# Kernel tuning notes

Measured on AMD Instinct MI355X. Metric: run time of the kernel, lower is better.

Reference implementation:

```python
import jax, jax.numpy as jnp
import numpy as np

NUM_Q = 8
DIM = 256
N_EMBED = 1024
COMMITMENT = 1.0


def setup_inputs() -> dict:
    key = jax.random.key(0)
    kx, ke = jax.random.split(key)
    x = jax.random.normal(kx, (32, 2048, DIM), dtype=jnp.float32)
    # one codebook per residual layer, stored as [dim, n_embed] like torch buffer `embed`
    embeds = jax.random.normal(ke, (NUM_Q, DIM, N_EMBED), dtype=jnp.float32)
    return {"x": x, "embeds": embeds}


def _vq_layer(residual, embed):
    # residual: [B, T, D]; embed: [D, K]
    flat = residual.reshape(-1, DIM)                                   # [N, D]
    dist = (jnp.sum(flat * flat, axis=1, keepdims=True)
            - 2.0 * flat @ embed
            + jnp.sum(embed * embed, axis=0, keepdims=True))           # [N, K]
    ind = jnp.argmin(dist, axis=1)                                     # [N]
    quantize = jnp.take(embed.T, ind, axis=0).reshape(residual.shape)  # [B, T, D]
    # commitment loss: mse(stopgrad(quantize), input)
    loss = jnp.mean((jax.lax.stop_gradient(quantize) - residual) ** 2) * COMMITMENT
    # straight-through estimator
    quantize_st = residual + jax.lax.stop_gradient(quantize - residual)
    # perplexity from code usage histogram
    counts = jnp.zeros((N_EMBED,), dtype=flat.dtype).at[ind].add(1.0)
    avg_probs = counts / flat.shape[0]
    perplexity = jnp.exp(-jnp.sum(avg_probs * jnp.log(avg_probs + 1e-10)))
    return quantize_st, loss, perplexity


def reference(x, embeds):
    def step(carry, embed):
        residual, quantized_out = carry
        q, loss, perp = _vq_layer(residual, embed)
        return (residual - q, quantized_out + q), (loss, perp)

    init = (x, jnp.zeros_like(x))
    (residual, quantized_out), (losses, perps) = jax.lax.scan(step, init, embeds)
    return quantized_out, losses, perps
```

## Files before the change

kernel.cpp:

```cpp
#include <hip/hip_runtime.h>
#include <math.h>
#include <stdint.h>

#define NQ 8
#define DIMV 256
#define KCODES 1024
#define NTOK 65536
#define NELEM (NTOK * DIMV)
#define TOKPB 64

typedef _Float16 f16x8 __attribute__((ext_vector_type(8)));
typedef float    f32x16 __attribute__((ext_vector_type(16)));

__device__ __forceinline__ int rotl3(int s) { return ((s << 3) | (s >> 2)) & 31; }

__global__ __launch_bounds__(256)
void vq_transpose(const float* __restrict__ embeds, float* __restrict__ embedT) {
    const int idx = blockIdx.x * 256 + threadIdx.x;
    const int q   = idx >> 18;
    const int rem = idx & 262143;
    const int k   = rem >> 8;
    const int d   = rem & 255;
    embedT[idx] = embeds[q * 262144 + d * 1024 + k];
}

__global__ __launch_bounds__(256)
void vq_e2(const float* __restrict__ embeds, float* __restrict__ e2) {
    const int idx = blockIdx.x * 256 + threadIdx.x;
    const int q = idx >> 10;
    const int k = idx & 1023;
    const float* e = embeds + q * 262144 + k;
    float s = 0.f;
    for (int d = 0; d < DIMV; ++d) {
        const float v = e[d * 1024];
        s += v * v;
    }
    e2[idx] = s;
}

__global__ __launch_bounds__(256)
void vq_embedB(const float* __restrict__ embeds, _Float16* __restrict__ embedB) {
    const int idx = blockIdx.x * 256 + threadIdx.x;
    const int j    = idx & 7;
    const int s    = (idx >> 3) & 127;
    const int part = (idx >> 10) & 1;
    const int w    = (idx >> 11) & 15;
    const int c    = (idx >> 15) & 15;
    const int q    = idx >> 19;
    const int h  = s >> 6;
    const int cl = s & 63;
    const int d  = c * 16 + h * 8 + j;
    const int k  = w * 64 + cl;
    const float v = embeds[q * 262144 + d * 1024 + k];
    const _Float16 hi = (_Float16)v;
    embedB[idx] = (part == 0) ? hi : (_Float16)(v - (float)hi);
}

#define LDS_BYTES 74080

__global__ __launch_bounds__(512, 4)
void vq_fused(const float* __restrict__ x, float* __restrict__ out,
              const float* __restrict__ embedT, const float* __restrict__ e2,
              const _Float16* __restrict__ embedB,
              float* __restrict__ lossSum, int* __restrict__ counts) {
    extern __shared__ char smem[];
    _Float16* Ahi = (_Float16*)smem;
    _Float16* Alo = (_Float16*)(smem + 32768);
    float* bestS   = (float*)(smem + 65536);
    int*   bestI   = (int*)(smem + 67616);
    int*   indF    = (int*)(smem + 69696);
    float* lossRed = (float*)(smem + 69952);
    float* e2Lds   = (float*)(smem + 69984);

    const int tid    = threadIdx.x;
    const int wave   = tid >> 6;
    const int lane   = tid & 63;
    const int l32    = lane & 31;
    const int h32    = lane >> 5;
    const int tok0   = blockIdx.x * TOKPB;

#pragma unroll
    for (int k = 0; k < 4; ++k) {
        const int si = tid + k * 512;
        const int t  = si >> 5;
        const int s  = si & 31;
        const float4 v0 = *(const float4*)(x + (tok0 + t) * 256 + s * 8);
        const float4 v1 = *(const float4*)(x + (tok0 + t) * 256 + s * 8 + 4);
        const float vv[8] = {v0.x, v0.y, v0.z, v0.w, v1.x, v1.y, v1.z, v1.w};
        f16x8 h8, l8;
#pragma unroll
        for (int e = 0; e < 8; ++e) {
            const _Float16 hi = (_Float16)vv[e];
            h8[e] = hi;
            l8[e] = (_Float16)(vv[e] - (float)hi);
        }
        const int ss = rotl3(s) ^ (t & 31);
        ((f16x8*)(Ahi + t * 256))[ss] = h8;
        ((f16x8*)(Alo + t * 256))[ss] = l8;
    }

#pragma unroll 1
    for (int q = 0; q < NQ; ++q) {
        const _Float16* embedBq = embedB + q * 524288;
        const float*    embedTq = embedT + q * (KCODES * DIMV);

        e2Lds[tid]       = e2[q * KCODES + tid];
        e2Lds[tid + 512] = e2[q * KCODES + tid + 512];
        __syncthreads();

        float bsv0 = 3.4e38f, bsv1 = 3.4e38f;
        int   biv0 = 0x7fffffff, biv1 = 0x7fffffff;

#pragma unroll
        for (int p = 0; p < 4; ++p) {
            f32x16 acc[2];
#pragma unroll
            for (int tt = 0; tt < 2; ++tt)
#pragma unroll
                for (int r = 0; r < 16; ++r) acc[tt][r] = 0.f;

            const char* gBp = (const char*)embedBq + (2 * wave + (p >> 1)) * 4096
                              + (p & 1) * 512 + h32 * 1024 + l32 * 16;

            f16x8 bH[3], bL[3];
            bH[0] = *(const f16x8*)(gBp);
            bL[0] = *(const f16x8*)(gBp + 2048);
            bH[1] = *(const f16x8*)(gBp + 65536);
            bL[1] = *(const f16x8*)(gBp + 65536 + 2048);

#pragma unroll
            for (int c = 0; c < 16; ++c) {
                const int cs = c % 3;
                if (c < 14) {
                    const char* gBn = gBp + (c + 2) * 65536;
                    bH[(c + 2) % 3] = *(const f16x8*)(gBn);
                    bL[(c + 2) % 3] = *(const f16x8*)(gBn + 2048);
                }
                f16x8 aH[2], aL[2];
#pragma unroll
                for (int tt = 0; tt < 2; ++tt) {
                    const int t  = tt * 32 + l32;
                    const int ss = rotl3(2 * c + h32) ^ l32;
                    aH[tt] = ((const f16x8*)(Ahi + t * 256))[ss];
                    aL[tt] = ((const f16x8*)(Alo + t * 256))[ss];
                }
#pragma unroll
                for (int tt = 0; tt < 2; ++tt) {
                    acc[tt] = __builtin_amdgcn_mfma_f32_32x32x16_f16(
                        bH[cs], aH[tt], acc[tt], 0, 0, 0);
                    acc[tt] = __builtin_amdgcn_mfma_f32_32x32x16_f16(
                        bL[cs], aH[tt], acc[tt], 0, 0, 0);
                    acc[tt] = __builtin_amdgcn_mfma_f32_32x32x16_f16(
                        bH[cs], aL[tt], acc[tt], 0, 0, 0);
                }
            }

#pragma unroll
            for (int tt = 0; tt < 2; ++tt) {
                float bs = (tt == 0) ? bsv0 : bsv1;
                int   bi = (tt == 0) ? biv0 : biv1;
#pragma unroll
                for (int r = 0; r < 16; ++r) {
                    const int cd = wave * 128 + p * 32 + (r & 3) + 8 * (r >> 2) + 4 * h32;
                    const float sc = e2Lds[cd] - 2.0f * acc[tt][r];
                    if (sc < bs || (sc == bs && cd < bi)) { bs = sc; bi = cd; }
                }
                if (tt == 0) { bsv0 = bs; biv0 = bi; } else { bsv1 = bs; biv1 = bi; }
            }
        }

#pragma unroll
        for (int tt = 0; tt < 2; ++tt) {
            float bs = (tt == 0) ? bsv0 : bsv1;
            int   bi = (tt == 0) ? biv0 : biv1;
            const float so = __shfl_xor(bs, 32);
            const int   io = __shfl_xor(bi, 32);
            if (so < bs || (so == bs && io < bi)) { bs = so; bi = io; }
            if (h32 == 0) {
                bestS[wave * 65 + tt * 32 + l32] = bs;
                bestI[wave * 65 + tt * 32 + l32] = bi;
            }
        }
        __syncthreads();

        {
            const int t = tid >> 3;
            const int g = tid & 7;
            float bs = bestS[g * 65 + t];
            int   bi = bestI[g * 65 + t];
#pragma unroll
            for (int m = 1; m < 8; m <<= 1) {
                const float so = __shfl_xor(bs, m);
                const int   io = __shfl_xor(bi, m);
                if (so < bs || (so == bs && io < bi)) { bs = so; bi = io; }
            }
            if (g == 0) {
                indF[t] = bi;
                atomicAdd(&counts[q * KCODES + bi], 1);
            }
        }
        __syncthreads();

        {
            const int tl = tid >> 3;
            const int sg = tid & 7;
            const int csel = indF[tl];
            const float* gq = embedTq + csel * 256;
            float lp = 0.f;
            f16x8* rowH = (f16x8*)(Ahi + tl * 256);
            f16x8* rowL = (f16x8*)(Alo + tl * 256);
#pragma unroll
            for (int it = 0; it < 4; ++it) {
                const int slotIdx = sg * 4 + it;
                const int slot = rotl3(slotIdx) ^ (tl & 31);
                f16x8 h8 = rowH[slot];
                f16x8 l8 = rowL[slot];
                const float4 q0 = *(const float4*)(gq + slotIdx * 8);
                const float4 q1 = *(const float4*)(gq + slotIdx * 8 + 4);
                const float qv[8] = {q0.x, q0.y, q0.z, q0.w, q1.x, q1.y, q1.z, q1.w};
#pragma unroll
                for (int e = 0; e < 8; ++e) {
                    const float rv = (float)h8[e] + (float)l8[e];
                    const float nr = rv - qv[e];
                    lp += nr * nr;
                    const _Float16 nh = (_Float16)nr;
                    h8[e] = nh;
                    l8[e] = (_Float16)(nr - (float)nh);
                }
                rowH[slot] = h8;
                rowL[slot] = l8;
            }
#pragma unroll
            for (int off = 32; off > 0; off >>= 1) lp += __shfl_down(lp, off);
            if (lane == 0) lossRed[wave] = lp;
        }
        __syncthreads();
        if (tid < 64) {
            float v = (lane < 8) ? lossRed[lane] : 0.f;
#pragma unroll
            for (int off = 4; off > 0; off >>= 1) v += __shfl_down(v, off);
            if (lane == 0) atomicAdd(lossSum + q, v);
        }
    }

#pragma unroll
    for (int k = 0; k < 4; ++k) {
        const int si = tid + k * 512;
        const int t  = si >> 5;
        const int s  = si & 31;
        const int ss = rotl3(s) ^ (t & 31);
        const f16x8 h8 = ((const f16x8*)(Ahi + t * 256))[ss];
        const f16x8 l8 = ((const f16x8*)(Alo + t * 256))[ss];
        const float4 x0 = *(const float4*)(x + (tok0 + t) * 256 + s * 8);
        const float4 x1 = *(const float4*)(x + (tok0 + t) * 256 + s * 8 + 4);
        float4 o0, o1;
        o0.x = x0.x - ((float)h8[0] + (float)l8[0]);
        o0.y = x0.y - ((float)h8[1] + (float)l8[1]);
        o0.z = x0.z - ((float)h8[2] + (float)l8[2]);
        o0.w = x0.w - ((float)h8[3] + (float)l8[3]);
        o1.x = x1.x - ((float)h8[4] + (float)l8[4]);
        o1.y = x1.y - ((float)h8[5] + (float)l8[5]);
        o1.z = x1.z - ((float)h8[6] + (float)l8[6]);
        o1.w = x1.w - ((float)h8[7] + (float)l8[7]);
        *(float4*)(out + (tok0 + t) * 256 + s * 8)     = o0;
        *(float4*)(out + (tok0 + t) * 256 + s * 8 + 4) = o1;
    }
}

__global__ __launch_bounds__(256)
void vq_finalize(const int* __restrict__ counts, const float* __restrict__ lossSum,
                 float* __restrict__ outTail) {
    const int q = blockIdx.x;
    const int tid = threadIdx.x;
    float s = 0.f;
    for (int k = tid; k < KCODES; k += 256) {
        const float p = (float)counts[q * KCODES + k] * (1.0f / 65536.0f);
        s += p * logf(p + 1e-10f);
    }
    for (int off = 32; off > 0; off >>= 1) s += __shfl_down(s, off);
    __shared__ float wpart[4];
    if ((tid & 63) == 0) wpart[tid >> 6] = s;
    __syncthreads();
    if (tid == 0) {
        outTail[q]     = lossSum[q] * (1.0f / 16777216.0f);
        outTail[8 + q] = expf(-(wpart[0] + wpart[1] + wpart[2] + wpart[3]));
    }
}

extern "C" void kernel_launch(void* const* d_in, const int* in_sizes, int n_in,
                              void* d_out, int out_size, void* d_ws, size_t ws_size,
                              hipStream_t stream) {
    const float* x      = (const float*)d_in[0];
    const float* embeds = (const float*)d_in[1];
    float* out = (float*)d_out;

    float* embedT   = (float*)d_ws;
    float* e2       = embedT + 2097152;
    float* lossSum  = e2 + 8192;
    int*   counts   = (int*)(lossSum + 8);
    _Float16* embedB = (_Float16*)(counts + 8192);

    hipMemsetAsync(lossSum, 0, (8 + 8192) * sizeof(float), stream);

    vq_transpose<<<8192, 256, 0, stream>>>(embeds, embedT);
    vq_e2<<<32, 256, 0, stream>>>(embeds, e2);
    vq_embedB<<<16384, 256, 0, stream>>>(embeds, embedB);

    hipFuncSetAttribute((const void*)vq_fused,
                        hipFuncAttributeMaxDynamicSharedMemorySize, LDS_BYTES);
    vq_fused<<<NTOK / TOKPB, 512, LDS_BYTES, stream>>>(
        x, out, embedT, e2, embedB, lossSum, counts);

    vq_finalize<<<NQ, 256, 0, stream>>>(counts, lossSum, out + NELEM);
}
```

Measured before the change: 1.189 ms.

## Merge argmin and residual-update phases, deepen B prefetch, remap block order

```diff
diff --git a/kernel.cpp b/kernel.cpp
--- a/kernel.cpp
+++ b/kernel.cpp
@@ -56,7 +56,7 @@
     embedB[idx] = (part == 0) ? hi : (_Float16)(v - (float)hi);
 }
 
-#define LDS_BYTES 74080
+#define LDS_BYTES 73792
 
 __global__ __launch_bounds__(512, 4)
 void vq_fused(const float* __restrict__ x, float* __restrict__ out,
@@ -68,16 +68,16 @@
     _Float16* Alo = (_Float16*)(smem + 32768);
     float* bestS   = (float*)(smem + 65536);
     int*   bestI   = (int*)(smem + 67616);
-    int*   indF    = (int*)(smem + 69696);
-    float* lossRed = (float*)(smem + 69952);
-    float* e2Lds   = (float*)(smem + 69984);
+    float* e2Lds   = (float*)(smem + 69696);
 
     const int tid    = threadIdx.x;
     const int wave   = tid >> 6;
     const int lane   = tid & 63;
     const int l32    = lane & 31;
     const int h32    = lane >> 5;
-    const int tok0   = blockIdx.x * TOKPB;
+    const int bid0 = blockIdx.x;
+    const int bid  = ((bid0 & 7) << 7) | (bid0 >> 3);
+    const int tok0 = bid * TOKPB;
 
 #pragma unroll
     for (int k = 0; k < 4; ++k) {
@@ -122,19 +122,21 @@
             const char* gBp = (const char*)embedBq + (2 * wave + (p >> 1)) * 4096
                               + (p & 1) * 512 + h32 * 1024 + l32 * 16;
 
-            f16x8 bH[3], bL[3];
+            f16x8 bH[4], bL[4];
             bH[0] = *(const f16x8*)(gBp);
             bL[0] = *(const f16x8*)(gBp + 2048);
             bH[1] = *(const f16x8*)(gBp + 65536);
             bL[1] = *(const f16x8*)(gBp + 65536 + 2048);
+            bH[2] = *(const f16x8*)(gBp + 131072);
+            bL[2] = *(const f16x8*)(gBp + 131072 + 2048);
 
 #pragma unroll
             for (int c = 0; c < 16; ++c) {
-                const int cs = c % 3;
-                if (c < 14) {
-                    const char* gBn = gBp + (c + 2) * 65536;
-                    bH[(c + 2) % 3] = *(const f16x8*)(gBn);
-                    bL[(c + 2) % 3] = *(const f16x8*)(gBn + 2048);
+                const int cs = c & 3;
+                if (c < 13) {
+                    const char* gBn = gBp + (c + 3) * 65536;
+                    bH[(c + 3) & 3] = *(const f16x8*)(gBn);
+                    bL[(c + 3) & 3] = *(const f16x8*)(gBn + 2048);
                 }
                 f16x8 aH[2], aL[2];
 #pragma unroll
@@ -184,34 +186,25 @@
         __syncthreads();
 
         {
-            const int t = tid >> 3;
-            const int g = tid & 7;
-            float bs = bestS[g * 65 + t];
-            int   bi = bestI[g * 65 + t];
+            const int tl = tid >> 3;
+            const int g  = tid & 7;
+            float bs = bestS[g * 65 + tl];
+            int   bi = bestI[g * 65 + tl];
 #pragma unroll
             for (int m = 1; m < 8; m <<= 1) {
                 const float so = __shfl_xor(bs, m);
                 const int   io = __shfl_xor(bi, m);
                 if (so < bs || (so == bs && io < bi)) { bs = so; bi = io; }
             }
-            if (g == 0) {
-                indF[t] = bi;
-                atomicAdd(&counts[q * KCODES + bi], 1);
-            }
-        }
-        __syncthreads();
-
-        {
-            const int tl = tid >> 3;
-            const int sg = tid & 7;
-            const int csel = indF[tl];
-            const float* gq = embedTq + csel * 256;
+            if (g == 0) atomicAdd(&counts[q * KCODES + bi], 1);
+
+            const float* gq = embedTq + bi * 256;
             float lp = 0.f;
             f16x8* rowH = (f16x8*)(Ahi + tl * 256);
             f16x8* rowL = (f16x8*)(Alo + tl * 256);
 #pragma unroll
             for (int it = 0; it < 4; ++it) {
-                const int slotIdx = sg * 4 + it;
+                const int slotIdx = g * 4 + it;
                 const int slot = rotl3(slotIdx) ^ (tl & 31);
                 f16x8 h8 = rowH[slot];
                 f16x8 l8 = rowL[slot];
@@ -232,16 +225,11 @@
             }
 #pragma unroll
             for (int off = 32; off > 0; off >>= 1) lp += __shfl_down(lp, off);
-            if (lane == 0) lossRed[wave] = lp;
+            if (lane == 0) atomicAdd(lossSum + q, lp);
         }
-        __syncthreads();
-        if (tid < 64) {
-            float v = (lane < 8) ? lossRed[lane] : 0.f;
-#pragma unroll
-            for (int off = 4; off > 0; off >>= 1) v += __shfl_down(v, off);
-            if (lane == 0) atomicAdd(lossSum + q, v);
-        }
-    }
+    }
+
+    __syncthreads();
 
 #pragma unroll
     for (int k = 0; k < 4; ++k) {
```

Result: slower. 1.368 ms (+15.0%).
